# Kernel tuning notes

Hardware: AMD Instinct MI355X
Metric: run time of the kernel (lower is better)

The kernel has to match this reference:

```python
import jax, jax.numpy as jnp
import numpy as np

B, S, D = 4, 2048, 1024
H = 16
HD = D // H  # 64
ROPE_BASE = 10000.0


def _rope_cache(seq_len, dim, dtype=jnp.float32):
    inv_freq = 1.0 / (ROPE_BASE ** (jnp.arange(0, dim, 2, dtype=jnp.float32) / dim))
    t = jnp.arange(seq_len, dtype=jnp.float32)
    freqs = jnp.outer(t, inv_freq)            # [S, dim/2]
    emb = jnp.concatenate([freqs, freqs], -1)  # [S, dim]
    return jnp.cos(emb).astype(dtype), jnp.sin(emb).astype(dtype)


def _rotate_half(x):
    x1, x2 = jnp.split(x, 2, axis=-1)
    return jnp.concatenate([-x2, x1], axis=-1)


def setup_inputs() -> dict:
    key = jax.random.key(0)
    k1, k2, k3 = jax.random.split(key, 3)
    x = jax.random.normal(k1, (B, S, D), dtype=jnp.float32)
    attention_mask = jnp.ones((B, S), dtype=jnp.int32)
    # torch nn.Linear weight is [out, in]; we store [in, out] for x @ W
    w_qkv = jax.random.normal(k2, (D, 3 * D), dtype=jnp.float32) * (1.0 / np.sqrt(D))
    w_out = jax.random.normal(k3, (D, D), dtype=jnp.float32) * (1.0 / np.sqrt(D))
    return {"x": x, "attention_mask": attention_mask, "w_qkv": w_qkv, "w_out": w_out}


def reference(x, attention_mask, w_qkv, w_out):
    b, s, d = x.shape
    qkv = x @ w_qkv                                  # [B,S,3D]
    qkv = qkv.reshape(b, s, 3, H, HD)
    q, k, v = [jnp.transpose(qkv[:, :, i], (0, 2, 1, 3)) for i in range(3)]  # [B,H,S,HD]
    cos, sin = _rope_cache(s, HD, x.dtype)           # [S,HD]
    cos = cos[None, None]                            # [1,1,S,HD]
    sin = sin[None, None]
    q = q * cos + _rotate_half(q) * sin
    k = k * cos + _rotate_half(k) * sin
    scale = 1.0 / np.sqrt(HD)
    scores = jnp.einsum("bhqd,bhkd->bhqk", q, k) * scale  # [B,H,S,S]
    causal = jnp.triu(jnp.ones((s, s), dtype=bool), k=1)
    neg_inf = jnp.finfo(scores.dtype).min
    scores = jnp.where(causal[None, None], -jnp.inf, scores)
    pad = (attention_mask == 0)[:, None, None, :]    # [B,1,1,S]
    scores = jnp.where(pad, -jnp.inf, scores)
    attn = jax.nn.softmax(scores, axis=-1)
    out = jnp.einsum("bhqk,bhkd->bhqd", attn, v)     # [B,H,S,HD]
    out = jnp.transpose(out, (0, 2, 1, 3)).reshape(b, s, d)
    return out @ w_out
```

## Files before the change

### kernel.cpp

```cpp
#include <hip/hip_runtime.h>

#define BQ 4
#define SQ 2048
#define DQ 1024
#define HQ 16
#define BHQ 64

typedef __attribute__((ext_vector_type(8))) short short8;
typedef __attribute__((ext_vector_type(4))) float f32x4;
typedef __attribute__((ext_vector_type(16))) float f32x16;
typedef __attribute__((ext_vector_type(2))) unsigned int u32x2;
typedef unsigned short u16;
typedef unsigned int u32;
typedef unsigned long long u64;

__device__ __forceinline__ u16 f2bf(float f) {
  u32 u = __float_as_uint(f);
  u32 r = u + 0x7fffu + ((u >> 16) & 1u);
  return (u16)(r >> 16);
}
__device__ __forceinline__ float bf2f(u16 h) {
  return __uint_as_float(((u32)h) << 16);
}

__device__ __forceinline__ u32 pkbf(float lo, float hi_) {
  u32 r;
  asm("v_cvt_pk_bf16_f32 %0, %1, %2" : "=v"(r) : "v"(lo), "v"(hi_));
  return r;
}
__device__ __forceinline__ float fexp2(float x) {
  float r;
  asm("v_exp_f32 %0, %1" : "=v"(r) : "v"(x));
  return r;
}
__device__ __forceinline__ float xmax32(float x) { return fmaxf(x, __shfl_xor(x, 32)); }
__device__ __forceinline__ float xsum32(float x) { return x + __shfl_xor(x, 32); }
__device__ __forceinline__ void pswap(u32& a, u32& b) {
  u32x2 r = __builtin_amdgcn_permlane32_swap(a, b, false, false);
  a = r.x;
  b = r.y;
}

__device__ __forceinline__ void gload_lds16(const void* g, void* l) {
  __builtin_amdgcn_global_load_lds(
      (const __attribute__((address_space(1))) u32*)(unsigned long long)g,
      (__attribute__((address_space(3))) u32*)(u32)(unsigned long long)l,
      16, 0, 0);
}

__device__ __forceinline__ void transpose_body(const float* __restrict__ in, u16* __restrict__ out,
                                               int R, int C, int bx, int by, int tid) {
  __shared__ float t[32][33];
  int c0 = bx * 32, r0 = by * 32;
  int tx = tid & 31, ty = tid >> 5;
  for (int rr = ty; rr < 32; rr += 8)
    t[rr][tx] = in[(size_t)(r0 + rr) * C + c0 + tx];
  __syncthreads();
  for (int rr = ty; rr < 32; rr += 8)
    out[(size_t)(c0 + rr) * R + r0 + tx] = f2bf(t[tx][rr]);
}

__global__ __launch_bounds__(256) void k_prep(const float* __restrict__ x, u16* __restrict__ xb,
                                              const float* __restrict__ wqkv, u16* __restrict__ wqkvT,
                                              const float* __restrict__ wout, u16* __restrict__ woutT,
                                              float* __restrict__ tab, const int* __restrict__ mask,
                                              u64* __restrict__ mbits) {
  int bid = blockIdx.x, tid = threadIdx.x;
  if (bid < 8192) {
    int i = bid * 256 + tid;
    float4 v = ((const float4*)x)[i];
    ushort4 o;
    o.x = f2bf(v.x); o.y = f2bf(v.y); o.z = f2bf(v.z); o.w = f2bf(v.w);
    ((ushort4*)xb)[i] = o;
  } else if (bid < 11264) {
    int t = bid - 8192;
    transpose_body(wqkv, wqkvT, 1024, 3072, t % 96, t / 96, tid);
  } else if (bid < 12288) {
    int t = bid - 11264;
    transpose_body(wout, woutT, 1024, 1024, t % 32, t / 32, tid);
  } else if (bid < 12544) {
    int i = (bid - 12288) * 256 + tid;
    int s = i >> 5, dp = i & 31;
    float invf = expf(-0.28782313662425576f * (float)dp);
    float ang = (float)s * invf;
    tab[i * 2] = cosf(ang);
    tab[i * 2 + 1] = sinf(ang);
  } else {
    int b = tid >> 6, c = tid & 63;
    int all1 = 1;
    for (int i = 0; i < 32; ++i) all1 &= (mask[b * SQ + c * 32 + i] != 0) ? 1 : 0;
    u64 m = __ballot(all1);
    if (c == 0) mbits[b] = m;
  }
}

template <int EPI>
__global__ __launch_bounds__(256) void k_gemm(const u16* __restrict__ A, const u16* __restrict__ Bt,
                                              float* __restrict__ Cf, u16* __restrict__ qb,
                                              u16* __restrict__ kb, u16* __restrict__ vTs,
                                              const float* __restrict__ tab, int K) {
  __shared__ u16 lA[128 * 64];
  __shared__ u16 lB[128 * 64];
  int bid = blockIdx.x;
  int i_ = bid >> 3;
  int tm = (bid & 7) * 8 + (i_ & 7);
  int tn = i_ >> 3;
  int tid = threadIdx.x, w = tid >> 6, l = tid & 63;
  int wm = w >> 1, wn = w & 1;
  int li = l & 15, lg = l >> 4;
  const u16* gA = A + (size_t)tm * 128 * K;
  const u16* gB = Bt + (size_t)tn * 128 * K;
  f32x4 acc[4][4];
#pragma unroll
  for (int i = 0; i < 4; i++)
#pragma unroll
    for (int j = 0; j < 4; j++) acc[i][j] = (f32x4){0.f, 0.f, 0.f, 0.f};

  int lr = l >> 3, lslot = l & 7;
  int scol = ((lslot ^ lr) * 8);

  for (int kt = 0; kt < K; kt += 64) {
    __syncthreads();
#pragma unroll
    for (int i = 0; i < 4; ++i) {
      int ch = i * 4 + w;
      int row = ch * 8 + lr;
      gload_lds16(gA + (size_t)row * K + kt + scol, &lA[ch * 512]);
      gload_lds16(gB + (size_t)row * K + kt + scol, &lB[ch * 512]);
    }
    __syncthreads();
#pragma unroll
    for (int kk = 0; kk < 2; ++kk) {
      short8 af[4], bfr[4];
#pragma unroll
      for (int mf = 0; mf < 4; ++mf) {
        int row = wm * 64 + mf * 16 + li;
        af[mf] = *(const short8*)&lA[row * 64 + (((kk * 4 + lg)) ^ (row & 7)) * 8];
      }
#pragma unroll
      for (int nf = 0; nf < 4; ++nf) {
        int row = wn * 64 + nf * 16 + li;
        bfr[nf] = *(const short8*)&lB[row * 64 + (((kk * 4 + lg)) ^ (row & 7)) * 8];
      }
#pragma unroll
      for (int mf = 0; mf < 4; ++mf)
#pragma unroll
        for (int nf = 0; nf < 4; ++nf)
          acc[mf][nf] = __builtin_amdgcn_mfma_f32_16x16x32_bf16(af[mf], bfr[nf], acc[mf][nf], 0, 0, 0);
    }
  }
  if (EPI == 0) {
#pragma unroll
    for (int mf = 0; mf < 4; ++mf) {
      int mg0 = tm * 128 + wm * 64 + mf * 16 + lg * 4;
#pragma unroll
      for (int nf = 0; nf < 4; ++nf) {
        int ng = tn * 128 + wn * 64 + nf * 16 + li;
#pragma unroll
        for (int r = 0; r < 4; ++r)
          Cf[(size_t)(mg0 + r) * 1024 + ng] = acc[mf][nf][r];
      }
    }
  } else {
    int which = tn >> 3;
    int h = (tn & 7) * 2 + wn;
    int b = tm >> 4;
    if (which < 2) {
      float scale = (which == 0) ? 0.125f * 1.44269504088896f : 1.0f;
      u16* qk0 = qb + (((size_t)b * HQ + h) * SQ << 6);
      u16* kb0 = kb + ((size_t)b * HQ + h) * (64 * 2048);
#pragma unroll
      for (int mf = 0; mf < 4; ++mf) {
#pragma unroll
        for (int r = 0; r < 4; ++r) {
          int s = (tm * 128 + wm * 64 + mf * 16 + lg * 4 + r) & 2047;
#pragma unroll
          for (int nf2 = 0; nf2 < 2; ++nf2) {
            int dp = nf2 * 16 + li;
            float2 cs = *(const float2*)&tab[(s * 32 + dp) * 2];
            float a = acc[mf][nf2][r];
            float bb = acc[mf][nf2 + 2][r];
            float lo = (a * cs.x - bb * cs.y) * scale;
            float hi2 = (bb * cs.x + a * cs.y) * scale;
            if (which == 0) {
              u16* dst = qk0 + ((size_t)s << 6);
              dst[dp] = f2bf(lo);
              dst[dp + 32] = f2bf(hi2);
            } else {
              u16* dst = kb0 + (s >> 5) * 2048 + (s & 31) * 8;
              dst[(dp >> 3) * 256 + (dp & 7)] = f2bf(lo);
              dst[(dp >> 3) * 256 + 1024 + (dp & 7)] = f2bf(hi2);
            }
          }
        }
      }
    } else {
#pragma unroll
      for (int mf = 0; mf < 4; ++mf) {
        int s0 = (tm * 128 + wm * 64 + mf * 16 + lg * 4) & 2047;
        int kt = s0 >> 5, kk0 = s0 & 31;
        size_t tb = (((size_t)(b * HQ + h) * 64 + kt) * 2048) + (kk0 >> 3) * 512 + (kk0 & 7);
#pragma unroll
        for (int nf = 0; nf < 4; ++nf) {
          int d = nf * 16 + li;
          u32 w0 = pkbf(acc[mf][nf][0], acc[mf][nf][1]);
          u32 w1 = pkbf(acc[mf][nf][2], acc[mf][nf][3]);
          *(u32x2*)&vTs[tb + d * 8] = (u32x2){w0, w1};
        }
      }
    }
  }
}

__global__ __launch_bounds__(256) void k_flash12(const u16* __restrict__ Q, const u16* __restrict__ Kb,
                                                 const u16* __restrict__ VTs, const int* __restrict__ mask,
                                                 const u64* __restrict__ mbits, u16* __restrict__ O) {
  __shared__ alignas(16) u16 Kl[2][4096];
  __shared__ alignas(16) u16 Vl[2][4096];
  int bid = blockIdx.x;
  int bh = bid & 63;
  int u = bid >> 6, v = u & 3, k4 = u >> 2;
  int qsup = (k4 == 0) ? v : (k4 == 1) ? 7 - v : (k4 == 2) ? 8 + v : 15 - v;
  int tid = threadIdx.x, w = tid >> 6, l = tid & 63;
  int j = l & 31, hi = l >> 5;
  int myqt = qsup * 4 + w;
  int P = 2 * qsup + 2;
  int b = bh >> 4, h = bh & 15;
  const int* mp = mask + b * SQ + 4 * hi;
  u64 mb = mbits[b];

  const u16* Kg0 = Kb + (size_t)bh * (64 * 2048) + tid * 8;
  const u16* Vg0 = VTs + (size_t)bh * (64 * 2048) + tid * 8;
  u16* KlB = &Kl[0][(size_t)w * 512];
  u16* VlB = &Vl[0][(size_t)w * 512];

  int qbase = myqt * 32;
  const u16* qp = Q + ((size_t)bh * SQ + qbase + j) * 64 + hi * 8;
  short8 qf[4];
#pragma unroll
  for (int kb = 0; kb < 4; ++kb) qf[kb] = *(const short8*)(qp + kb * 16);

  f32x16 o0, o1;
#pragma unroll
  for (int i = 0; i < 16; ++i) { o0[i] = 0.f; o1[i] = 0.f; }
  float mrun = -INFINITY, lrun = 0.f;

  gload_lds16(Kg0, KlB);
  gload_lds16(Kg0 + 2048, KlB + 2048);
  gload_lds16(Vg0, VlB);
  gload_lds16(Vg0 + 2048, VlB + 2048);
  __syncthreads();

  for (int ph = 0; ph < P; ++ph) {
    int cur = ph & 1;
    if (ph + 1 < P) {
      const u16* kg = Kg0 + (size_t)(2 * ph + 2) * 2048;
      const u16* vg = Vg0 + (size_t)(2 * ph + 2) * 2048;
      u16* kd = KlB + (cur ^ 1) * 4096;
      u16* vd = VlB + (cur ^ 1) * 4096;
      gload_lds16(kg, kd);
      gload_lds16(kg + 2048, kd + 2048);
      gload_lds16(vg, vd);
      gload_lds16(vg + 2048, vd + 2048);
    }

#pragma unroll
    for (int sub = 0; sub < 2; ++sub) {
      int kt = 2 * ph + sub;
      if (kt <= myqt) {
        const u16* Kc = &Kl[cur][sub * 2048];
        const u16* Vc = &Vl[cur][sub * 2048];

        short8 kcf[4];
#pragma unroll
        for (int kb = 0; kb < 4; ++kb)
          kcf[kb] = *(const short8*)&Kc[(hi + 2 * kb) * 256 + j * 8];

        f32x16 s;
#pragma unroll
        for (int i = 0; i < 16; ++i) s[i] = 0.f;
        __builtin_amdgcn_s_setprio(1);
#pragma unroll
        for (int kb = 0; kb < 4; ++kb)
          s = __builtin_amdgcn_mfma_f32_32x32x16_bf16(kcf[kb], qf[kb], s, 0, 0, 0);
        __builtin_amdgcn_s_setprio(0);

        short8 va0 = *(const short8*)&Vc[hi * 512 + j * 8];
        short8 va1 = *(const short8*)&Vc[(hi + 2) * 512 + j * 8];
        short8 vb0 = *(const short8*)&Vc[hi * 512 + (j + 32) * 8];
        short8 vb1 = *(const short8*)&Vc[(hi + 2) * 512 + (j + 32) * 8];

        if (!((mb >> kt) & 1ull)) {
#pragma unroll
          for (int rq = 0; rq < 4; ++rq) {
            int4 mv = *(const int4*)(mp + kt * 32 + 8 * rq);
            if (!mv.x) s[4 * rq + 0] = -INFINITY;
            if (!mv.y) s[4 * rq + 1] = -INFINITY;
            if (!mv.z) s[4 * rq + 2] = -INFINITY;
            if (!mv.w) s[4 * rq + 3] = -INFINITY;
          }
        }
        if (kt == myqt) {
#pragma unroll
          for (int rq = 0; rq < 4; ++rq)
#pragma unroll
            for (int t = 0; t < 4; ++t)
              if (8 * rq + 4 * hi + t > j) s[4 * rq + t] = -INFINITY;
        }

        float t0 = fmaxf(fmaxf(fmaxf(s[0], s[1]), fmaxf(s[2], s[3])),
                         fmaxf(fmaxf(s[4], s[5]), fmaxf(s[6], s[7])));
        t0 = fmaxf(t0, fmaxf(fmaxf(fmaxf(s[8], s[9]), fmaxf(s[10], s[11])),
                             fmaxf(fmaxf(s[12], s[13]), fmaxf(s[14], s[15]))));
        if (!__all(t0 <= mrun + 8.0f)) {
          float tm2 = xmax32(t0);
          float mn = fmaxf(fmaxf(mrun, tm2), -1e30f);
          float alpha = fexp2(mrun - mn);
          mrun = mn;
          lrun *= alpha;
#pragma unroll
          for (int i = 0; i < 16; ++i) { o0[i] *= alpha; o1[i] *= alpha; }
        }
        float ts = 0.f;
#pragma unroll
        for (int i = 0; i < 16; ++i) {
          float pv = fexp2(s[i] - mrun);
          s[i] = pv;
          ts += pv;
        }
        lrun += ts;

        u32 pa[4], pb[4];
#pragma unroll
        for (int q2 = 0; q2 < 4; ++q2) {
          pa[q2] = pkbf(s[4 * q2 + 0], s[4 * q2 + 1]);
          pb[q2] = pkbf(s[4 * q2 + 2], s[4 * q2 + 3]);
        }
        pswap(pa[0], pa[1]);
        pswap(pb[0], pb[1]);
        pswap(pa[2], pa[3]);
        pswap(pb[2], pb[3]);
        union { short8 s8; u32 wd[4]; } f0, f1;
        f0.wd[0] = pa[0];
        f0.wd[1] = pb[0];
        f0.wd[2] = pa[1];
        f0.wd[3] = pb[1];
        f1.wd[0] = pa[2];
        f1.wd[1] = pb[2];
        f1.wd[2] = pa[3];
        f1.wd[3] = pb[3];

        __builtin_amdgcn_s_setprio(1);
        o0 = __builtin_amdgcn_mfma_f32_32x32x16_bf16(va0, f0.s8, o0, 0, 0, 0);
        o0 = __builtin_amdgcn_mfma_f32_32x32x16_bf16(va1, f1.s8, o0, 0, 0, 0);
        o1 = __builtin_amdgcn_mfma_f32_32x32x16_bf16(vb0, f0.s8, o1, 0, 0, 0);
        o1 = __builtin_amdgcn_mfma_f32_32x32x16_bf16(vb1, f1.s8, o1, 0, 0, 0);
        __builtin_amdgcn_s_setprio(0);
      }
    }

    __syncthreads();
  }

  float lfull = xsum32(lrun);
  float inv = 1.0f / lfull;
  u16* ob = O + ((size_t)b * SQ + qbase + j) * DQ + h * 64 + 4 * hi;
#pragma unroll
  for (int q2 = 0; q2 < 4; ++q2) {
#pragma unroll
    for (int e = 0; e < 2; ++e) {
      *(u32*)(ob + 8 * q2 + 2 * e) = pkbf(o0[4 * q2 + 2 * e] * inv, o0[4 * q2 + 2 * e + 1] * inv);
      *(u32*)(ob + 32 + 8 * q2 + 2 * e) = pkbf(o1[4 * q2 + 2 * e] * inv, o1[4 * q2 + 2 * e + 1] * inv);
    }
  }
}

extern "C" void kernel_launch(void* const* d_in, const int* in_sizes, int n_in,
                              void* d_out, int out_size, void* d_ws, size_t ws_size,
                              hipStream_t stream) {
  const float* x = (const float*)d_in[0];
  const int* mask = (const int*)d_in[1];
  const float* wqkv = (const float*)d_in[2];
  const float* wout = (const float*)d_in[3];
  float* out = (float*)d_out;
  char* ws = (char*)d_ws;

  u16* xb    = (u16*)(ws + 0);
  u16* wqkvT = (u16*)(ws + 16777216);
  u16* woutT = (u16*)(ws + 23068672);
  u16* qbuf  = (u16*)(ws + 25165824);
  u16* kbuf  = (u16*)(ws + 41943040);
  u16* vTs   = (u16*)(ws + 75497472);
  u16* attnb = (u16*)(ws + 92274688);
  float* tab = (float*)(ws + 109051904);
  u64* mbits = (u64*)(ws + 109576192);

  k_prep<<<12545, 256, 0, stream>>>(x, xb, wqkv, wqkvT, wout, woutT, tab, mask, mbits);
  k_gemm<1><<<1536, 256, 0, stream>>>(xb, wqkvT, nullptr, qbuf, kbuf, vTs, tab, 1024);
  k_flash12<<<1024, 256, 0, stream>>>(qbuf, kbuf, vTs, mask, mbits, attnb);
  k_gemm<0><<<512, 256, 0, stream>>>(attnb, woutT, out, nullptr, nullptr, nullptr, nullptr, 1024);
}
```

Measured before the change: 183.5 us.

## Double-buffer GEMM LDS tiles with K=32 stages and prefetch next tile

Restructures the projection GEMM main loop from a single 64-wide K tile with two barriers per step into a double-buffered 32-wide K pipeline. The next tile is issued to LDS while MFMAs run on the current one, leaving one barrier per iteration, and the swizzle moves from 8-way to 4-way XOR. MFMA sections are bracketed with s_setprio to favor math issue. This doubles the iteration count and halves the work per barrier, so the overlap gain could be offset by loop overhead or by changed LDS bank-conflict behavior.

```diff
diff --git a/kernel.cpp b/kernel.cpp
--- a/kernel.cpp
+++ b/kernel.cpp
@@ -99,8 +99,8 @@
                                               float* __restrict__ Cf, u16* __restrict__ qb,
                                               u16* __restrict__ kb, u16* __restrict__ vTs,
                                               const float* __restrict__ tab, int K) {
-  __shared__ u16 lA[128 * 64];
-  __shared__ u16 lB[128 * 64];
+  __shared__ u16 lA[2][128 * 32];
+  __shared__ u16 lB[2][128 * 32];
   int bid = blockIdx.x;
   int i_ = bid >> 3;
   int tm = (bid & 7) * 8 + (i_ & 7);
@@ -116,39 +116,56 @@
 #pragma unroll
     for (int j = 0; j < 4; j++) acc[i][j] = (f32x4){0.f, 0.f, 0.f, 0.f};
 
-  int lr = l >> 3, lslot = l & 7;
-  int scol = ((lslot ^ lr) * 8);
-
-  for (int kt = 0; kt < K; kt += 64) {
+  int sl0 = tid, sl1 = tid + 256;
+  int r0_ = sl0 >> 2, c0_ = ((sl0 & 3) ^ (r0_ & 3)) * 8;
+  int r1_ = sl1 >> 2, c1_ = ((sl1 & 3) ^ (r1_ & 3)) * 8;
+  const u16* aS0 = gA + (size_t)r0_ * K + c0_;
+  const u16* aS1 = gA + (size_t)r1_ * K + c1_;
+  const u16* bS0 = gB + (size_t)r0_ * K + c0_;
+  const u16* bS1 = gB + (size_t)r1_ * K + c1_;
+  u16* aD0 = &lA[0][w * 64 * 8];
+  u16* bD0 = &lB[0][w * 64 * 8];
+
+  int NT = K >> 5;
+  gload_lds16(aS0, aD0);
+  gload_lds16(aS1, aD0 + 2048);
+  gload_lds16(bS0, bD0);
+  gload_lds16(bS1, bD0 + 2048);
+  __syncthreads();
+
+  for (int t = 0; t < NT; ++t) {
+    int cur = t & 1;
+    if (t + 1 < NT) {
+      int off = (t + 1) * 32;
+      int bo = (cur ^ 1) * 4096;
+      gload_lds16(aS0 + off, aD0 + bo);
+      gload_lds16(aS1 + off, aD0 + bo + 2048);
+      gload_lds16(bS0 + off, bD0 + bo);
+      gload_lds16(bS1 + off, bD0 + bo + 2048);
+    }
+    const u16* As = lA[cur];
+    const u16* Bs = lB[cur];
+    short8 af[4], bfr[4];
+#pragma unroll
+    for (int mf = 0; mf < 4; ++mf) {
+      int row = wm * 64 + mf * 16 + li;
+      af[mf] = *(const short8*)&As[row * 32 + (lg ^ (row & 3)) * 8];
+    }
+#pragma unroll
+    for (int nf = 0; nf < 4; ++nf) {
+      int row = wn * 64 + nf * 16 + li;
+      bfr[nf] = *(const short8*)&Bs[row * 32 + (lg ^ (row & 3)) * 8];
+    }
+    __builtin_amdgcn_s_setprio(1);
+#pragma unroll
+    for (int mf = 0; mf < 4; ++mf)
+#pragma unroll
+      for (int nf = 0; nf < 4; ++nf)
+        acc[mf][nf] = __builtin_amdgcn_mfma_f32_16x16x32_bf16(af[mf], bfr[nf], acc[mf][nf], 0, 0, 0);
+    __builtin_amdgcn_s_setprio(0);
     __syncthreads();
-#pragma unroll
-    for (int i = 0; i < 4; ++i) {
-      int ch = i * 4 + w;
-      int row = ch * 8 + lr;
-      gload_lds16(gA + (size_t)row * K + kt + scol, &lA[ch * 512]);
-      gload_lds16(gB + (size_t)row * K + kt + scol, &lB[ch * 512]);
-    }
-    __syncthreads();
-#pragma unroll
-    for (int kk = 0; kk < 2; ++kk) {
-      short8 af[4], bfr[4];
-#pragma unroll
-      for (int mf = 0; mf < 4; ++mf) {
-        int row = wm * 64 + mf * 16 + li;
-        af[mf] = *(const short8*)&lA[row * 64 + (((kk * 4 + lg)) ^ (row & 7)) * 8];
-      }
-#pragma unroll
-      for (int nf = 0; nf < 4; ++nf) {
-        int row = wn * 64 + nf * 16 + li;
-        bfr[nf] = *(const short8*)&lB[row * 64 + (((kk * 4 + lg)) ^ (row & 7)) * 8];
-      }
-#pragma unroll
-      for (int mf = 0; mf < 4; ++mf)
-#pragma unroll
-        for (int nf = 0; nf < 4; ++nf)
-          acc[mf][nf] = __builtin_amdgcn_mfma_f32_16x16x32_bf16(af[mf], bfr[nf], acc[mf][nf], 0, 0, 0);
-    }
   }
+
   if (EPI == 0) {
 #pragma unroll
     for (int mf = 0; mf < 4; ++mf) {
```

After: 181.7 us. No clear change (-1.0%).
